# Kernel optimization log

Measured on AMD Instinct MI355X. Metric: run time of the kernel, lower is better.

## Reference

```python
import jax, jax.numpy as jnp
import numpy as np

B, N, H = 32, 512, 128
LN_EPS = 1e-5

def _layernorm(x):
    # LayerNorm over last dim, no affine (elementwise_affine=False)
    mu = jnp.mean(x, axis=-1, keepdims=True)
    var = jnp.var(x, axis=-1, keepdims=True)
    return (x - mu) * jax.lax.rsqrt(var + LN_EPS)

def setup_inputs() -> dict:
    key = jax.random.key(0)
    k0, k1, k2, k3 = jax.random.split(key, 4)
    s = jax.random.normal(k0, (B, N, H), dtype=jnp.float32)
    ev = jax.random.normal(k1, (B, N, N, 3), dtype=jnp.float32)
    mask = (jax.random.uniform(k2, (B, N, N, 1)) > 0.5).astype(jnp.float32)
    W1 = jax.random.normal(k3, (H, H), dtype=jnp.float32) / np.sqrt(H)
    b1 = jnp.zeros((H,), dtype=jnp.float32)
    return {"s": s, "ev": ev, "mask": mask, "W1": W1, "b1": b1}

def reference(s, ev, mask, W1, b1):
    # lin1: Linear -> LayerNorm (no affine) -> SiLU
    h = jnp.einsum('bnh,kh->bnk', s, W1) + b1          # (B, N, H)
    h = jax.nn.silu(_layernorm(h))
    # Fused CFConv: v[b,i,c,d] = sum_j mask[b,i,j] * ev[b,i,j,c] * h[b,j,d]
    mev = ev * mask                                     # (B, N, N, 3)
    v = jnp.einsum('bijc,bjd->bicd', mev, h)            # (B, N, 3, H)
    return v
```

## Files before the change

kernel.cpp:

```cpp
#include <hip/hip_runtime.h>
#include <hip/hip_bf16.h>

#define B_ 32
#define N_ 512
#define H_ 128

typedef float f32x4 __attribute__((ext_vector_type(4)));
typedef short short8 __attribute__((ext_vector_type(8)));
typedef short short4v __attribute__((ext_vector_type(4)));

static __device__ __forceinline__ float bf2f(unsigned short u) {
  union { unsigned int ui; float f; } x;
  x.ui = ((unsigned int)u) << 16;
  return x.f;
}
static __device__ __forceinline__ unsigned short f2bf(float f) {
  __hip_bfloat16 h = __float2bfloat16(f);
  return *reinterpret_cast<unsigned short*>(&h);
}

__global__ __launch_bounds__(256) void lin_ln_silu_kernel(
    const float* __restrict__ s, const float* __restrict__ W1,
    const float* __restrict__ b1, unsigned short* __restrict__ h_t) {
  __shared__ float s_sh[32 * 132];
  __shared__ unsigned short w_sh[128 * 132];
  __shared__ unsigned short ht_sh[128 * 40];
  const int t = threadIdx.x;
  const int b = blockIdx.y;
  const int n0 = blockIdx.x * 32;

#pragma unroll
  for (int r = 0; r < 16; ++r) {
    int q = t + 256 * r;
    int d = q >> 5, part = q & 31;
    float4 v = *reinterpret_cast<const float4*>(W1 + d * H_ + part * 4);
    short4v w;
    w.x = (short)f2bf(v.x); w.y = (short)f2bf(v.y);
    w.z = (short)f2bf(v.z); w.w = (short)f2bf(v.w);
    *reinterpret_cast<short4v*>(&w_sh[d * 132 + part * 4]) = w;
  }
#pragma unroll
  for (int r = 0; r < 4; ++r) {
    int q = t + 256 * r;
    int n = q >> 5, part = q & 31;
    float4 v = *reinterpret_cast<const float4*>(
        s + ((size_t)b * N_ + n0 + n) * H_ + part * 4);
    *reinterpret_cast<float4*>(&s_sh[n * 132 + part * 4]) = v;
  }
  __syncthreads();

  const int a = t & 15;
  const int g = t >> 4;
  float acc[2][8];
#pragma unroll
  for (int nn = 0; nn < 2; ++nn)
#pragma unroll
    for (int dd = 0; dd < 8; ++dd) acc[nn][dd] = 0.f;

  float bias[8];
#pragma unroll
  for (int dd = 0; dd < 8; ++dd) bias[dd] = b1[dd * 16 + a];

  for (int k = 0; k < 128; k += 4) {
    float wf[8][4];
#pragma unroll
    for (int dd = 0; dd < 8; ++dd) {
      short4v wv =
          *reinterpret_cast<const short4v*>(&w_sh[(dd * 16 + a) * 132 + k]);
      wf[dd][0] = bf2f((unsigned short)wv.x);
      wf[dd][1] = bf2f((unsigned short)wv.y);
      wf[dd][2] = bf2f((unsigned short)wv.z);
      wf[dd][3] = bf2f((unsigned short)wv.w);
    }
#pragma unroll
    for (int nn = 0; nn < 2; ++nn) {
      float4 sv =
          *reinterpret_cast<const float4*>(&s_sh[(nn * 16 + g) * 132 + k]);
#pragma unroll
      for (int dd = 0; dd < 8; ++dd) {
        acc[nn][dd] += sv.x * wf[dd][0] + sv.y * wf[dd][1] +
                       sv.z * wf[dd][2] + sv.w * wf[dd][3];
      }
    }
  }

#pragma unroll
  for (int nn = 0; nn < 2; ++nn) {
    float s1 = 0.f, s2 = 0.f;
#pragma unroll
    for (int dd = 0; dd < 8; ++dd) {
      float x = acc[nn][dd] + bias[dd];
      acc[nn][dd] = x;
      s1 += x;
      s2 += x * x;
    }
#pragma unroll
    for (int off = 8; off >= 1; off >>= 1) {
      s1 += __shfl_xor(s1, off);
      s2 += __shfl_xor(s2, off);
    }
    float mean = s1 * (1.f / 128.f);
    float var = s2 * (1.f / 128.f) - mean * mean;
    float rs = rsqrtf(var + 1e-5f);
#pragma unroll
    for (int dd = 0; dd < 8; ++dd) {
      float x = (acc[nn][dd] - mean) * rs;
      float y = x / (1.f + __expf(-x));
      ht_sh[(dd * 16 + a) * 40 + nn * 16 + g] = f2bf(y);
    }
  }
  __syncthreads();

#pragma unroll
  for (int r = 0; r < 2; ++r) {
    int q = t + 256 * r;
    int d = q >> 2, part = q & 3;
    float4 v = *reinterpret_cast<const float4*>(&ht_sh[d * 40 + part * 8]);
    *reinterpret_cast<float4*>(
        h_t + ((size_t)b * 128 + d) * 512 + n0 + part * 8) = v;
  }
}

__global__ __launch_bounds__(256) void cfconv_mfma_kernel(
    const float* __restrict__ ev, const float* __restrict__ mask,
    const unsigned short* __restrict__ h_t, float* __restrict__ out) {
  __shared__ unsigned short ph[48 * 72];
  __shared__ unsigned short hh[128 * 72];
  const int t = threadIdx.x;
  const int b = blockIdx.y;
  const int i0 = blockIdx.x * 16;
  const int lane = t & 63;
  const int w = t >> 6;
  const int l15 = lane & 15;
  const int quad = lane >> 4;

  f32x4 acc[3][2];
#pragma unroll
  for (int mt = 0; mt < 3; ++mt)
#pragma unroll
    for (int nt = 0; nt < 2; ++nt)
#pragma unroll
      for (int e = 0; e < 4; ++e) acc[mt][nt][e] = 0.f;

  for (int j0 = 0; j0 < N_; j0 += 64) {
    __syncthreads();

#pragma unroll
    for (int r = 0; r < 4; ++r) {
      int q = t + 256 * r;
      int d = q >> 3, p8 = q & 7;
      float4 v = *reinterpret_cast<const float4*>(
          h_t + ((size_t)b * 128 + d) * 512 + j0 + p8 * 8);
      *reinterpret_cast<float4*>(&hh[d * 72 + p8 * 8]) = v;
    }

#pragma unroll
    for (int r = 0; r < 3; ++r) {
      int q = t + 256 * r;
      int i = q / 48, part = q % 48;
      int f0 = part * 4;
      const float* evbase =
          ev + ((size_t)((b * N_ + i0 + i)) * N_ + j0) * 3;
      float4 e4 = *reinterpret_cast<const float4*>(evbase + f0);
      const float* mrow = mask + (size_t)(b * N_ + i0 + i) * N_ + j0;
      int jlo = f0 / 3, jhi = (f0 + 3) / 3;
      float mlo = mrow[jlo], mhi = mrow[jhi];
      float evv[4] = {e4.x, e4.y, e4.z, e4.w};
#pragma unroll
      for (int e = 0; e < 4; ++e) {
        int f = f0 + e;
        int j = f / 3, c = f - 3 * j;
        float m = (j == jlo) ? mlo : mhi;
        ph[(c * 16 + i) * 72 + j] = f2bf(evv[e] * m);
      }
    }
    __syncthreads();

#pragma unroll
    for (int ks = 0; ks < 2; ++ks) {
      short8 av[3], bv[2];
#pragma unroll
      for (int mt = 0; mt < 3; ++mt)
        av[mt] = *reinterpret_cast<const short8*>(
            &ph[(mt * 16 + l15) * 72 + ks * 32 + quad * 8]);
#pragma unroll
      for (int nt = 0; nt < 2; ++nt) {
        int d = w * 32 + nt * 16 + l15;
        bv[nt] = *reinterpret_cast<const short8*>(
            &hh[d * 72 + ks * 32 + quad * 8]);
      }
#pragma unroll
      for (int mt = 0; mt < 3; ++mt)
#pragma unroll
        for (int nt = 0; nt < 2; ++nt)
          acc[mt][nt] = __builtin_amdgcn_mfma_f32_16x16x32_bf16(
              av[mt], bv[nt], acc[mt][nt], 0, 0, 0);
    }
  }

#pragma unroll
  for (int mt = 0; mt < 3; ++mt) {
#pragma unroll
    for (int nt = 0; nt < 2; ++nt) {
      int d = w * 32 + nt * 16 + l15;
#pragma unroll
      for (int r = 0; r < 4; ++r) {
        int i = i0 + quad * 4 + r;
        out[(((size_t)b * N_ + i) * 3 + mt) * H_ + d] = acc[mt][nt][r];
      }
    }
  }
}

extern "C" void kernel_launch(void* const* d_in, const int* in_sizes, int n_in,
                              void* d_out, int out_size, void* d_ws,
                              size_t ws_size, hipStream_t stream) {
  const float* s = (const float*)d_in[0];
  const float* ev = (const float*)d_in[1];
  const float* mask = (const float*)d_in[2];
  const float* W1 = (const float*)d_in[3];
  const float* b1 = (const float*)d_in[4];
  float* out = (float*)d_out;
  unsigned short* h_t = (unsigned short*)d_ws;

  lin_ln_silu_kernel<<<dim3(N_ / 32, B_), 256, 0, stream>>>(s, W1, b1, h_t);
  cfconv_mfma_kernel<<<dim3(N_ / 16, B_), 256, 0, stream>>>(ev, mask, h_t, out);
}
```

Measured before the change: 212.2 us.

## Restructure CFConv to keep full h in LDS and double-buffer ev/mask loads in registers

Result: no change. 213.2 us (+0.5%).

```diff
diff --git a/kernel.cpp b/kernel.cpp
--- a/kernel.cpp
+++ b/kernel.cpp
@@ -121,91 +121,129 @@
   }
 }
 
-__global__ __launch_bounds__(256) void cfconv_mfma_kernel(
+__global__ __launch_bounds__(256, 1) void cfconv_mfma_kernel(
     const float* __restrict__ ev, const float* __restrict__ mask,
     const unsigned short* __restrict__ h_t, float* __restrict__ out) {
-  __shared__ unsigned short ph[48 * 72];
-  __shared__ unsigned short hh[128 * 72];
+  __shared__ unsigned short hL[128 * 512];
   const int t = threadIdx.x;
   const int b = blockIdx.y;
-  const int i0 = blockIdx.x * 16;
-  const int lane = t & 63;
-  const int w = t >> 6;
-  const int l15 = lane & 15;
-  const int quad = lane >> 4;
-
-  f32x4 acc[3][2];
+  const int i0 = blockIdx.x * 64;
+  const int w = t >> 6, l = t & 63;
+  const int l15 = l & 15, quad = l >> 4;
+  const int ig = i0 + w * 16 + l15;
+
+  {
+    const unsigned short* hb = h_t + (size_t)b * 65536;
+#pragma unroll 4
+    for (int r2 = 0; r2 < 32; ++r2) {
+      int row = w * 32 + r2;
+      float4 v = *reinterpret_cast<const float4*>(hb + row * 512 + l * 8);
+      *reinterpret_cast<float4*>(
+          &hL[row * 512 + (l >> 3) * 64 + (((l & 7) ^ (row & 7)) * 8)]) = v;
+    }
+  }
+  __syncthreads();
+
+  f32x4 acc[3][8];
 #pragma unroll
   for (int mt = 0; mt < 3; ++mt)
 #pragma unroll
-    for (int nt = 0; nt < 2; ++nt)
+    for (int nt = 0; nt < 8; ++nt)
 #pragma unroll
       for (int e = 0; e < 4; ++e) acc[mt][nt][e] = 0.f;
 
-  for (int j0 = 0; j0 < N_; j0 += 64) {
-    __syncthreads();
-
-#pragma unroll
-    for (int r = 0; r < 4; ++r) {
-      int q = t + 256 * r;
-      int d = q >> 3, p8 = q & 7;
-      float4 v = *reinterpret_cast<const float4*>(
-          h_t + ((size_t)b * 128 + d) * 512 + j0 + p8 * 8);
-      *reinterpret_cast<float4*>(&hh[d * 72 + p8 * 8]) = v;
-    }
-
-#pragma unroll
-    for (int r = 0; r < 3; ++r) {
-      int q = t + 256 * r;
-      int i = q / 48, part = q % 48;
-      int f0 = part * 4;
-      const float* evbase =
-          ev + ((size_t)((b * N_ + i0 + i)) * N_ + j0) * 3;
-      float4 e4 = *reinterpret_cast<const float4*>(evbase + f0);
-      const float* mrow = mask + (size_t)(b * N_ + i0 + i) * N_ + j0;
-      int jlo = f0 / 3, jhi = (f0 + 3) / 3;
-      float mlo = mrow[jlo], mhi = mrow[jhi];
-      float evv[4] = {e4.x, e4.y, e4.z, e4.w};
-#pragma unroll
-      for (int e = 0; e < 4; ++e) {
-        int f = f0 + e;
-        int j = f / 3, c = f - 3 * j;
-        float m = (j == jlo) ? mlo : mhi;
-        ph[(c * 16 + i) * 72 + j] = f2bf(evv[e] * m);
-      }
-    }
-    __syncthreads();
-
-#pragma unroll
-    for (int ks = 0; ks < 2; ++ks) {
-      short8 av[3], bv[2];
-#pragma unroll
-      for (int mt = 0; mt < 3; ++mt)
-        av[mt] = *reinterpret_cast<const short8*>(
-            &ph[(mt * 16 + l15) * 72 + ks * 32 + quad * 8]);
-#pragma unroll
-      for (int nt = 0; nt < 2; ++nt) {
-        int d = w * 32 + nt * 16 + l15;
-        bv[nt] = *reinterpret_cast<const short8*>(
-            &hh[d * 72 + ks * 32 + quad * 8]);
-      }
-#pragma unroll
-      for (int mt = 0; mt < 3; ++mt)
-#pragma unroll
-        for (int nt = 0; nt < 2; ++nt)
-          acc[mt][nt] = __builtin_amdgcn_mfma_f32_16x16x32_bf16(
-              av[mt], bv[nt], acc[mt][nt], 0, 0, 0);
-    }
-  }
+  const float* evrow =
+      ev + ((size_t)(b * N_) + ig) * (N_ * 3) + quad * 24;
+  const float* mrow = mask + ((size_t)(b * N_) + ig) * N_ + quad * 8;
+
+  f32x4 evA[12], mkA[4], evB[12], mkB[4];
+  short8 av[3][2];
+
+#define ALOADO(DST, PTR, OFF)                                    \
+  asm volatile("global_load_dwordx4 %0, %1, off offset:" OFF     \
+               : "=v"(DST) : "v"(PTR))
+
+#define ISSUE_SET(EVX, MKX, R)                                   \
+  do {                                                           \
+    const char* ep_ = (const char*)evrow + (R)*768;              \
+    const char* mp_ = (const char*)mrow + (R)*256;               \
+    ALOADO(EVX[0], ep_, "0");    ALOADO(EVX[1], ep_, "16");      \
+    ALOADO(EVX[2], ep_, "32");   ALOADO(EVX[3], ep_, "48");      \
+    ALOADO(EVX[4], ep_, "64");   ALOADO(EVX[5], ep_, "80");      \
+    ALOADO(EVX[6], ep_, "384");  ALOADO(EVX[7], ep_, "400");     \
+    ALOADO(EVX[8], ep_, "416");  ALOADO(EVX[9], ep_, "432");     \
+    ALOADO(EVX[10], ep_, "448"); ALOADO(EVX[11], ep_, "464");    \
+    ALOADO(MKX[0], mp_, "0");    ALOADO(MKX[1], mp_, "16");      \
+    ALOADO(MKX[2], mp_, "128");  ALOADO(MKX[3], mp_, "144");     \
+  } while (0)
+
+#define VMW(n)                                       \
+  do {                                               \
+    asm volatile("s_waitcnt vmcnt(" #n ")");         \
+    __builtin_amdgcn_sched_barrier(0);               \
+  } while (0)
+
+#define CONV(EVX, MKX)                                                  \
+  do {                                                                  \
+    _Pragma("unroll") for (int ks_ = 0; ks_ < 2; ++ks_) {               \
+      float p_[8][3];                                                   \
+      _Pragma("unroll") for (int e_ = 0; e_ < 8; ++e_) {                \
+        float mv_ = MKX[ks_ * 2 + (e_ >> 2)][e_ & 3];                   \
+        _Pragma("unroll") for (int c_ = 0; c_ < 3; ++c_) {              \
+          int f_ = e_ * 3 + c_;                                         \
+          p_[e_][c_] = EVX[ks_ * 6 + (f_ >> 2)][f_ & 3] * mv_;          \
+        }                                                               \
+      }                                                                 \
+      _Pragma("unroll") for (int c_ = 0; c_ < 3; ++c_) {                \
+        short8 a_;                                                      \
+        _Pragma("unroll") for (int e_ = 0; e_ < 8; ++e_)                \
+            a_[e_] = (short)f2bf(p_[e_][c_]);                           \
+        av[c_][ks_] = a_;                                               \
+      }                                                                 \
+    }                                                                   \
+  } while (0)
+
+#define COMPUTE(J0)                                                     \
+  do {                                                                  \
+    _Pragma("unroll") for (int ks_ = 0; ks_ < 2; ++ks_) {               \
+      _Pragma("unroll") for (int nt_ = 0; nt_ < 8; ++nt_) {             \
+        int d_ = nt_ * 16 + l15;                                        \
+        short8 bv_ = *reinterpret_cast<const short8*>(                  \
+            &hL[d_ * 512 + (J0) +                                       \
+                (((ks_ * 4 + quad) ^ (l15 & 7)) * 8)]);                 \
+        _Pragma("unroll") for (int mt_ = 0; mt_ < 3; ++mt_)             \
+            acc[mt_][nt_] = __builtin_amdgcn_mfma_f32_16x16x32_bf16(    \
+                av[mt_][ks_], bv_, acc[mt_][nt_], 0, 0, 0);             \
+      }                                                                 \
+    }                                                                   \
+  } while (0)
+
+  ISSUE_SET(evA, mkA, 0);
+  ISSUE_SET(evB, mkB, 1);
+
+  VMW(16); CONV(evA, mkA); ISSUE_SET(evA, mkA, 2); COMPUTE(0);
+  VMW(16); CONV(evB, mkB); ISSUE_SET(evB, mkB, 3); COMPUTE(64);
+  VMW(16); CONV(evA, mkA); ISSUE_SET(evA, mkA, 4); COMPUTE(128);
+  VMW(16); CONV(evB, mkB); ISSUE_SET(evB, mkB, 5); COMPUTE(192);
+  VMW(16); CONV(evA, mkA); ISSUE_SET(evA, mkA, 6); COMPUTE(256);
+  VMW(16); CONV(evB, mkB); ISSUE_SET(evB, mkB, 7); COMPUTE(320);
+  VMW(16); CONV(evA, mkA); COMPUTE(384);
+  VMW(0);  CONV(evB, mkB); COMPUTE(448);
+
+#undef COMPUTE
+#undef CONV
+#undef VMW
+#undef ISSUE_SET
+#undef ALOADO
 
 #pragma unroll
   for (int mt = 0; mt < 3; ++mt) {
 #pragma unroll
-    for (int nt = 0; nt < 2; ++nt) {
-      int d = w * 32 + nt * 16 + l15;
+    for (int nt = 0; nt < 8; ++nt) {
+      int d = nt * 16 + l15;
 #pragma unroll
       for (int r = 0; r < 4; ++r) {
-        int i = i0 + quad * 4 + r;
+        int i = i0 + w * 16 + quad * 4 + r;
         out[(((size_t)b * N_ + i) * 3 + mt) * H_ + d] = acc[mt][nt][r];
       }
     }
@@ -224,5 +262,5 @@
   unsigned short* h_t = (unsigned short*)d_ws;
 
   lin_ln_silu_kernel<<<dim3(N_ / 32, B_), 256, 0, stream>>>(s, W1, b1, h_t);
-  cfconv_mfma_kernel<<<dim3(N_ / 16, B_), 256, 0, stream>>>(ev, mask, h_t, out);
-}
+  cfconv_mfma_kernel<<<dim3(N_ / 64, B_), 256, 0, stream>>>(ev, mask, h_t, out);
+}
```

## Rewrite CFConv as register-direct pipelined MFMA with split-K across two waves

Applied to the files above, without the earlier changes.

After: 218.0 us. 1.03x slower.

```diff
diff --git a/kernel.cpp b/kernel.cpp
--- a/kernel.cpp
+++ b/kernel.cpp
@@ -121,92 +121,147 @@
   }
 }
 
-__global__ __launch_bounds__(256) void cfconv_mfma_kernel(
+__global__ __launch_bounds__(128, 2) void cfconv_mfma_kernel(
     const float* __restrict__ ev, const float* __restrict__ mask,
     const unsigned short* __restrict__ h_t, float* __restrict__ out) {
-  __shared__ unsigned short ph[48 * 72];
-  __shared__ unsigned short hh[128 * 72];
+  __shared__ float red[64 * 98];
   const int t = threadIdx.x;
+  const int wv = t >> 6, l = t & 63;
+  const int l15 = l & 15, quad = l >> 4;
   const int b = blockIdx.y;
   const int i0 = blockIdx.x * 16;
-  const int lane = t & 63;
-  const int w = t >> 6;
-  const int l15 = lane & 15;
-  const int quad = lane >> 4;
-
-  f32x4 acc[3][2];
-#pragma unroll
-  for (int mt = 0; mt < 3; ++mt)
-#pragma unroll
-    for (int nt = 0; nt < 2; ++nt)
-#pragma unroll
-      for (int e = 0; e < 4; ++e) acc[mt][nt][e] = 0.f;
-
-  for (int j0 = 0; j0 < N_; j0 += 64) {
-    __syncthreads();
-
-#pragma unroll
-    for (int r = 0; r < 4; ++r) {
-      int q = t + 256 * r;
-      int d = q >> 3, p8 = q & 7;
-      float4 v = *reinterpret_cast<const float4*>(
-          h_t + ((size_t)b * 128 + d) * 512 + j0 + p8 * 8);
-      *reinterpret_cast<float4*>(&hh[d * 72 + p8 * 8]) = v;
-    }
-
-#pragma unroll
-    for (int r = 0; r < 3; ++r) {
-      int q = t + 256 * r;
-      int i = q / 48, part = q % 48;
-      int f0 = part * 4;
-      const float* evbase =
-          ev + ((size_t)((b * N_ + i0 + i)) * N_ + j0) * 3;
-      float4 e4 = *reinterpret_cast<const float4*>(evbase + f0);
-      const float* mrow = mask + (size_t)(b * N_ + i0 + i) * N_ + j0;
-      int jlo = f0 / 3, jhi = (f0 + 3) / 3;
-      float mlo = mrow[jlo], mhi = mrow[jhi];
-      float evv[4] = {e4.x, e4.y, e4.z, e4.w};
-#pragma unroll
-      for (int e = 0; e < 4; ++e) {
-        int f = f0 + e;
-        int j = f / 3, c = f - 3 * j;
-        float m = (j == jlo) ? mlo : mhi;
-        ph[(c * 16 + i) * 72 + j] = f2bf(evv[e] * m);
-      }
-    }
-    __syncthreads();
-
-#pragma unroll
-    for (int ks = 0; ks < 2; ++ks) {
-      short8 av[3], bv[2];
-#pragma unroll
-      for (int mt = 0; mt < 3; ++mt)
-        av[mt] = *reinterpret_cast<const short8*>(
-            &ph[(mt * 16 + l15) * 72 + ks * 32 + quad * 8]);
-#pragma unroll
-      for (int nt = 0; nt < 2; ++nt) {
-        int d = w * 32 + nt * 16 + l15;
-        bv[nt] = *reinterpret_cast<const short8*>(
-            &hh[d * 72 + ks * 32 + quad * 8]);
-      }
-#pragma unroll
-      for (int mt = 0; mt < 3; ++mt)
-#pragma unroll
-        for (int nt = 0; nt < 2; ++nt)
-          acc[mt][nt] = __builtin_amdgcn_mfma_f32_16x16x32_bf16(
-              av[mt], bv[nt], acc[mt][nt], 0, 0, 0);
-    }
-  }
-
-#pragma unroll
-  for (int mt = 0; mt < 3; ++mt) {
-#pragma unroll
-    for (int nt = 0; nt < 2; ++nt) {
-      int d = w * 32 + nt * 16 + l15;
-#pragma unroll
-      for (int r = 0; r < 4; ++r) {
-        int i = i0 + quad * 4 + r;
-        out[(((size_t)b * N_ + i) * 3 + mt) * H_ + d] = acc[mt][nt][r];
+  const int ig = i0 + l15;
+  const int j0 = wv * 256;
+
+  const char* evby = (const char*)ev +
+      (size_t)(b * N_ + ig) * 6144 + (size_t)(j0 + quad * 8) * 12;
+  const char* mby = (const char*)mask +
+      (size_t)(b * N_ + ig) * 2048 + (size_t)(j0 + quad * 8) * 4;
+  const char* hby[8];
+#pragma unroll
+  for (int nt = 0; nt < 8; ++nt)
+    hby[nt] = (const char*)h_t +
+        ((size_t)b * 65536 + (size_t)(nt * 16 + l15) * 512 +
+         (size_t)(j0 + quad * 8)) * 2;
+
+  f32x4 acc[3][8];
+#pragma unroll
+  for (int c = 0; c < 3; ++c)
+#pragma unroll
+    for (int nt = 0; nt < 8; ++nt)
+#pragma unroll
+      for (int e = 0; e < 4; ++e) acc[c][nt][e] = 0.f;
+
+  f32x4 evA[6], mkA[2], evB[6], mkB[2];
+  short8 bv[8];
+  short8 av[3];
+
+#define SB() __builtin_amdgcn_sched_barrier(0)
+#define ALOADF(DST, PTR, OFF)                                  \
+  asm volatile("global_load_dwordx4 %0, %1, off offset:" OFF   \
+               : "=v"(DST) : "v"(PTR))
+
+#define ISSUE_EVMK(EVX, MKX, R)                                \
+  do {                                                         \
+    const char* e_ = evby + (R) * 384;                         \
+    const char* m_ = mby + (R) * 128;                          \
+    ALOADF(EVX[0], e_, "0");  ALOADF(EVX[1], e_, "16");        \
+    ALOADF(EVX[2], e_, "32"); ALOADF(EVX[3], e_, "48");        \
+    ALOADF(EVX[4], e_, "64"); ALOADF(EVX[5], e_, "80");        \
+    ALOADF(MKX[0], m_, "0");  ALOADF(MKX[1], m_, "16");        \
+  } while (0)
+
+#define ISSUE_BV(R)                                            \
+  do {                                                         \
+    _Pragma("unroll") for (int nt_ = 0; nt_ < 8; ++nt_) {      \
+      const char* h_ = hby[nt_] + (R) * 64;                    \
+      ALOADF(bv[nt_], h_, "0");                                \
+    }                                                          \
+  } while (0)
+
+#define VMW(n)                                       \
+  do {                                               \
+    asm volatile("s_waitcnt vmcnt(" #n ")");         \
+    __builtin_amdgcn_sched_barrier(0);               \
+  } while (0)
+
+#define CONV(EVX, MKX)                                         \
+  do {                                                         \
+    _Pragma("unroll") for (int c_ = 0; c_ < 3; ++c_) {         \
+      short8 a_;                                               \
+      _Pragma("unroll") for (int e_ = 0; e_ < 8; ++e_) {       \
+        float mv_ = MKX[e_ >> 2][e_ & 3];                      \
+        int f_ = e_ * 3 + c_;                                  \
+        a_[e_] = (short)f2bf(EVX[f_ >> 2][f_ & 3] * mv_);      \
+      }                                                        \
+      av[c_] = a_;                                             \
+    }                                                          \
+  } while (0)
+
+#define COMPUTE()                                              \
+  do {                                                         \
+    _Pragma("unroll") for (int nt_ = 0; nt_ < 8; ++nt_)        \
+        _Pragma("unroll") for (int c_ = 0; c_ < 3; ++c_)       \
+            acc[c_][nt_] = __builtin_amdgcn_mfma_f32_16x16x32_bf16( \
+                av[c_], bv[nt_], acc[c_][nt_], 0, 0, 0);       \
+  } while (0)
+
+#define STEP(R, N1, N2, EVX, MKX)                              \
+  do {                                                         \
+    VMW(N1);                              \
+    CONV(EVX, MKX);                                            \
+    VMW(N2);                               \
+    COMPUTE();                                                 \
+    SB();                                                      \
+    if ((R) < 7) ISSUE_BV((R) + 1);                            \
+    if ((R) < 6) ISSUE_EVMK(EVX, MKX, (R) + 2);                \
+    SB();                                                      \
+  } while (0)
+
+  ISSUE_EVMK(evA, mkA, 0);
+  ISSUE_BV(0);
+  ISSUE_EVMK(evB, mkB, 1);
+
+  STEP(0, 16, 8, evA, mkA);
+  STEP(1, 16, 8, evB, mkB);
+  STEP(2, 16, 8, evA, mkA);
+  STEP(3, 16, 8, evB, mkB);
+  STEP(4, 16, 8, evA, mkA);
+  STEP(5, 16, 8, evB, mkB);
+  STEP(6, 16, 8, evA, mkA);
+  STEP(7, 8, 0, evB, mkB);
+
+#undef STEP
+#undef COMPUTE
+#undef CONV
+#undef VMW
+#undef ISSUE_BV
+#undef ISSUE_EVMK
+#undef ALOADF
+#undef SB
+
+  if (wv == 1) {
+#pragma unroll
+    for (int c = 0; c < 3; ++c)
+#pragma unroll
+      for (int nt = 0; nt < 8; ++nt)
+        *reinterpret_cast<f32x4*>(&red[l * 98 + (c * 8 + nt) * 4]) =
+            acc[c][nt];
+  }
+  __syncthreads();
+  if (wv == 0) {
+#pragma unroll
+    for (int c = 0; c < 3; ++c) {
+#pragma unroll
+      for (int nt = 0; nt < 8; ++nt) {
+        f32x4 o =
+            *reinterpret_cast<const f32x4*>(&red[l * 98 + (c * 8 + nt) * 4]);
+#pragma unroll
+        for (int r = 0; r < 4; ++r) {
+          int i = i0 + quad * 4 + r;
+          out[(((size_t)b * N_ + i) * 3 + c) * H_ + nt * 16 + l15] =
+              acc[c][nt][r] + o[r];
+        }
       }
     }
   }
@@ -224,5 +279,5 @@
   unsigned short* h_t = (unsigned short*)d_ws;
 
   lin_ln_silu_kernel<<<dim3(N_ / 32, B_), 256, 0, stream>>>(s, W1, b1, h_t);
-  cfconv_mfma_kernel<<<dim3(N_ / 16, B_), 256, 0, stream>>>(ev, mask, h_t, out);
-}
+  cfconv_mfma_kernel<<<dim3(N_ / 16, B_), 128, 0, stream>>>(ev, mask, h_t, out);
+}
```
